# Kernel optimization log

Measured on AMD Instinct MI355X. Metric: run time of the kernel, lower is better.

## Reference

```python
import jax, jax.numpy as jnp
import numpy as np


def _discretize(A, B, C, step):
    # Bilinear (Tustin) discretization, as in the source module.
    N = A.shape[0]
    I = jnp.eye(N, dtype=A.dtype)
    BL = jnp.linalg.inv(I - (step / 2.0) * A)
    Ab = BL @ (I + (step / 2.0) * A)
    Bb = (BL * step) @ B  # (N, 1)
    return Ab, Bb, C


def _k_conv(Ab, Bb, Cb, L):
    # K[l] = Cb @ Ab^l @ Bb, computed by a linear recurrence instead of
    # L explicit matrix powers (same math as the source's K_conv).
    def step(v, _):
        k = (Cb @ v)[0, 0]
        return Ab @ v, k

    _, K = jax.lax.scan(step, Bb, None, length=L)
    return K  # (L,)


def setup_inputs() -> dict:
    key = jax.random.key(0)
    k_u, k_a, k_b, k_c, k_s = jax.random.split(key, 5)
    N, L, BATCH = 64, 16384, 512
    u = jax.random.normal(k_u, (BATCH, L), dtype=jnp.float32)
    # lecun_normal inits: std = 1/sqrt(fan_in)
    A = jax.random.normal(k_a, (N, N), dtype=jnp.float32) / np.sqrt(N)
    B = jax.random.normal(k_b, (N, 1), dtype=jnp.float32)  # fan_in = 1
    C = jax.random.normal(k_c, (1, N), dtype=jnp.float32) / np.sqrt(N)
    D = jnp.ones((1,), dtype=jnp.float32)
    # log_step_initializer(dt_min=1e-3, dt_max=0.1)
    lo, hi = np.log(1e-3), np.log(0.1)
    log_step = (jax.random.uniform(k_s, (1,)) * (hi - lo) + lo).astype(jnp.float32)
    return {"u": u, "A": A, "B": B, "C": C, "D": D, "log_step": log_step}


def reference(u, A, B, C, D, log_step) -> jnp.ndarray:
    L = u.shape[-1]
    step = jnp.exp(log_step)  # (1,)
    Ab, Bb, Cb = _discretize(A, B, C, step)
    K = _k_conv(Ab, Bb, Cb, L)  # (L,)
    # FFT causal convolution: pad both signals to length 2L (as in source),
    # multiply in frequency domain, take first L samples.
    n = 2 * L
    ud = jnp.fft.rfft(u, n=n, axis=-1)          # (BATCH, L+1) complex
    Kd = jnp.fft.rfft(K, n=n)                   # (L+1,) complex, broadcast
    y = jnp.fft.irfft(ud * Kd, n=n, axis=-1)[..., :L]
    return y + D * u
```

## Files before the change

kernel.cpp:

```cpp
#include <hip/hip_runtime.h>
#include <cstddef>

typedef double f64x4 __attribute__((ext_vector_type(4)));
typedef float  f32x4 __attribute__((ext_vector_type(4)));
typedef short  bf16x8 __attribute__((ext_vector_type(8)));

static constexpr int RCN = 512 * 128;

static constexpr size_t WS_W  = 0;
static constexpr size_t WS_G  = 8192;
static constexpr size_t WS_MD = 32768;
static constexpr size_t WS_BV = 40960;
static constexpr size_t WS_X  = WS_BV + (size_t)RCN * 64;

__device__ __forceinline__ unsigned short f2bf(float f) {
  union { float f; unsigned u; } v; v.f = f;
  unsigned u = v.u + 0x7FFFu + ((v.u >> 16) & 1u);
  return (unsigned short)(u >> 16);
}

__device__ __forceinline__ double probeE(int i, int k) {
  return (double)(((i * 3 + k * 5) & 7) - 3);
}
__device__ __forceinline__ double probeF(int k, int j) {
  return (double)(((k * 7 + j * 2) & 7) - 4);
}

__device__ __forceinline__ bool probe_mfma_layout(int lr, int lq, int rowm[4], int* colm_out)
{
  f64x4 z; z[0] = 0.0; z[1] = 0.0; z[2] = 0.0; z[3] = 0.0;
  f64x4 p1 = __builtin_amdgcn_mfma_f64_16x16x4f64((double)lr, 1.0, z, 0, 0, 0);
  f64x4 p2 = __builtin_amdgcn_mfma_f64_16x16x4f64(1.0, (double)lr, z, 0, 0, 0);
  bool okl = true;
#pragma unroll
  for (int r = 0; r < 4; ++r) {
    int rr = (int)(p1[r] * 0.25 + 0.5);
    okl = okl && (p1[r] == 4.0 * (double)rr) && rr >= 0 && rr < 16;
    rowm[r] = rr & 15;
    okl = okl && (p2[r] == p2[0]);
  }
  int cc = (int)(p2[0] * 0.25 + 0.5);
  okl = okl && (p2[0] == 4.0 * (double)cc) && cc >= 0 && cc < 16;
  *colm_out = cc & 15;
  f64x4 d = __builtin_amdgcn_mfma_f64_16x16x4f64(probeE(lr, lq), probeF(lq, lr), z, 0, 0, 0);
#pragma unroll
  for (int r = 0; r < 4; ++r) {
    double ref = 0.0;
#pragma unroll
    for (int k = 0; k < 4; ++k) ref += probeE(rowm[r], k) * probeF(k, cc & 15);
    okl = okl && (d[r] == ref);
  }
  return __all(okl) != 0;
}

template<bool ADD>
__device__ __forceinline__ void mm64_mfma(const double* A, const double* B, double* D,
                                          int wi, int wj, int lr, int lq,
                                          const int rowm[4], int colm)
{
  f64x4 acc;
  if (ADD) {
#pragma unroll
    for (int r = 0; r < 4; ++r)
      acc[r] = D[(wi * 16 + rowm[r]) * 65 + wj * 16 + colm];
  } else {
    acc[0] = 0.0; acc[1] = 0.0; acc[2] = 0.0; acc[3] = 0.0;
  }
#pragma unroll
  for (int kb = 0; kb < 16; ++kb) {
    double a = A[(wi * 16 + lr) * 65 + kb * 4 + lq];
    double b = B[(kb * 4 + lq) * 65 + wj * 16 + lr];
    acc = __builtin_amdgcn_mfma_f64_16x16x4f64(a, b, acc, 0, 0, 0);
  }
  __syncthreads();
#pragma unroll
  for (int r = 0; r < 4; ++r)
    D[(wi * 16 + rowm[r]) * 65 + wj * 16 + colm] = acc[r];
  __syncthreads();
}

__device__ __forceinline__ void wh_tile(const float* Wf, const float* Hf,
                                        const double* Pd, float* Wo, float* Ho,
                                        int n, bool isW, int wi, int wj,
                                        int lr, int lq, const int rowm[4], int colm)
{
  f64x4 acc;
  acc[0] = 0.0; acc[1] = 0.0; acc[2] = 0.0; acc[3] = 0.0;
#pragma unroll
  for (int kb = 0; kb < 16; ++kb) {
    double a, b;
    if (isW) {
      a = (double)Wf[(wi * 16 + lr) * 65 + kb * 4 + lq];
      b = Pd[(wj * 16 + lr) * 65 + kb * 4 + lq];
    } else {
      a = (double)Hf[(wi * 16 + lr) * 65 + kb * 4 + lq];
      b = Pd[(kb * 4 + lq) * 65 + wj * 16 + lr];
    }
    acc = __builtin_amdgcn_mfma_f64_16x16x4f64(a, b, acc, 0, 0, 0);
  }
#pragma unroll
  for (int r = 0; r < 4; ++r) {
    int drow = wi * 16 + rowm[r];
    if (drow < n) {
      if (isW) Wo[(n + drow) * 65 + wj * 16 + colm] = (float)acc[r];
      else     Ho[(n + drow) * 65 + wj * 16 + colm] = (float)acc[r];
    }
  }
}

template<bool ADD>
__device__ __forceinline__ void mm64x2(const double* A, const double* B, double* D,
                                       int tr2, int tc2)
{
  double a00 = 0, a01 = 0, a10 = 0, a11 = 0;
#pragma unroll 8
  for (int c = 0; c < 64; ++c) {
    double av0 = A[(tr2 + 0) * 65 + c];
    double av1 = A[(tr2 + 1) * 65 + c];
    double bv0 = B[c * 65 + tc2 + 0];
    double bv1 = B[c * 65 + tc2 + 1];
    a00 = fma(av0, bv0, a00); a01 = fma(av0, bv1, a01);
    a10 = fma(av1, bv0, a10); a11 = fma(av1, bv1, a11);
  }
  double o00, o01, o10, o11;
  if (ADD) {
    o00 = D[(tr2 + 0) * 65 + tc2 + 0]; o01 = D[(tr2 + 0) * 65 + tc2 + 1];
    o10 = D[(tr2 + 1) * 65 + tc2 + 0]; o11 = D[(tr2 + 1) * 65 + tc2 + 1];
  }
  __syncthreads();
  D[(tr2 + 0) * 65 + tc2 + 0] = ADD ? (o00 + a00) : a00;
  D[(tr2 + 0) * 65 + tc2 + 1] = ADD ? (o01 + a01) : a01;
  D[(tr2 + 1) * 65 + tc2 + 0] = ADD ? (o10 + a10) : a10;
  D[(tr2 + 1) * 65 + tc2 + 1] = ADD ? (o11 + a11) : a11;
  __syncthreads();
}

__global__ __launch_bounds__(1024) void k_precomp(
    const float* __restrict__ Ain, const float* __restrict__ Bin,
    const float* __restrict__ Cin, const float* __restrict__ Din,
    const float* __restrict__ LS, float* ws)
{
  __shared__ double Xd[64 * 65];
  __shared__ double Pd[64 * 65];
  __shared__ float  Wf[128 * 65];
  __shared__ float  Hf[128 * 65];
  __shared__ float  Kf[128];

  const int t    = threadIdx.x;
  const int wave = t >> 6;
  const int lane = t & 63;
  const int lr   = lane & 15;
  const int lq   = lane >> 4;
  const int wv_i = wave >> 2;
  const int wv_j = wave & 3;
  const int tr2  = (t >> 5) << 1;
  const int tc2  = (t & 31) << 1;

  int rowm[4]; int colm;
  const bool use_mfma = probe_mfma_layout(lr, lq, rowm, &colm);

  unsigned short* Wtg = (unsigned short*)(ws + WS_W);
  unsigned short* Gtg = (unsigned short*)(ws + WS_G);
  float* Mf = ws + WS_MD;

  const double step = exp((double)LS[0]);
  const double h = 0.5 * step;

  for (int idx = t; idx < 4096; idx += 1024) {
    int i = idx >> 6, j = idx & 63;
    double a = h * (double)Ain[idx];
    Xd[i * 65 + j] = a;
    Pd[i * 65 + j] = a + ((i == j) ? 1.0 : 0.0);
  }
  __syncthreads();

  if (use_mfma) {
    for (int k = 0; k < 3; ++k) {
      mm64_mfma<false>(Xd, Xd, Xd, wv_i, wv_j, lr, lq, rowm, colm);
      mm64_mfma<true >(Pd, Xd, Pd, wv_i, wv_j, lr, lq, rowm, colm);
    }
  } else {
    for (int k = 0; k < 3; ++k) {
      mm64x2<false>(Xd, Xd, Xd, tr2, tc2);
      mm64x2<true >(Pd, Xd, Pd, tr2, tc2);
    }
  }

  if (t < 64) {
    double bb = 0.0;
    for (int c = 0; c < 64; ++c) bb = fma(Pd[t * 65 + c], (double)Bin[c], bb);
    Wf[t] = (float)(bb * step);
  }
  __syncthreads();

  for (int idx = t; idx < 4096; idx += 1024) {
    int i = idx >> 6, j = idx & 63;
    Pd[i * 65 + j] = 2.0 * Pd[i * 65 + j] - ((i == j) ? 1.0 : 0.0);
  }
  __syncthreads();

  if (t < 64) {
    double hh = 0.0;
    for (int c = 0; c < 64; ++c) hh = fma((double)Cin[c], Pd[c * 65 + t], hh);
    Hf[t] = (float)hh;
  }
  __syncthreads();

  if (use_mfma) {
    for (int k = 0; k < 7; ++k) {
      const int n     = 1 << k;
      const int tpm   = (n + 15) >> 4;
      const int tiles = tpm << 2;
      if (tiles <= 8) {
        if (wave < 2 * tiles) {
          const bool isW = wave < tiles;
          const int  w   = isW ? wave : wave - tiles;
          wh_tile(Wf, Hf, Pd, Wf, Hf, n, isW, w >> 2, w & 3, lr, lq, rowm, colm);
        }
      } else {
        wh_tile(Wf, Hf, Pd, Wf, Hf, n, true,  wv_i, wv_j, lr, lq, rowm, colm);
        wh_tile(Wf, Hf, Pd, Wf, Hf, n, false, wv_i, wv_j, lr, lq, rowm, colm);
      }
      mm64_mfma<false>(Pd, Pd, Pd, wv_i, wv_j, lr, lq, rowm, colm);
    }
  } else {
    for (int k = 0; k < 7; ++k) {
      const int n = 1 << k;
      if (n <= 16) {
        if (t < (n << 6)) {
          int r = t >> 6, ii = t & 63;
          double aw = 0.0, ah = 0.0;
#pragma unroll 4
          for (int c = 0; c < 64; ++c) {
            aw = fma(Pd[ii * 65 + c], (double)Wf[r * 65 + c], aw);
            ah = fma((double)Hf[r * 65 + c], Pd[c * 65 + ii], ah);
          }
          Wf[(n + r) * 65 + ii] = (float)aw;
          Hf[(n + r) * 65 + ii] = (float)ah;
        }
      } else if (n == 32) {
        const int r  = t >> 5;
        const int i2 = (t & 31) << 1;
        double w0 = 0, w1 = 0, h0 = 0, h1 = 0;
#pragma unroll 4
        for (int c = 0; c < 64; ++c) {
          double wr = (double)Wf[r * 65 + c];
          w0 = fma(wr, Pd[(i2 + 0) * 65 + c], w0);
          w1 = fma(wr, Pd[(i2 + 1) * 65 + c], w1);
          double hr = (double)Hf[r * 65 + c];
          h0 = fma(hr, Pd[c * 65 + i2 + 0], h0);
          h1 = fma(hr, Pd[c * 65 + i2 + 1], h1);
        }
        Wf[(32 + r) * 65 + i2 + 0] = (float)w0;
        Wf[(32 + r) * 65 + i2 + 1] = (float)w1;
        Hf[(32 + r) * 65 + i2 + 0] = (float)h0;
        Hf[(32 + r) * 65 + i2 + 1] = (float)h1;
      } else {
        const int r2 = tr2, i2 = tc2;
        double w00 = 0, w01 = 0, w10 = 0, w11 = 0;
        double h00 = 0, h01 = 0, h10 = 0, h11 = 0;
#pragma unroll 4
        for (int c = 0; c < 64; ++c) {
          double wa = (double)Wf[(r2 + 0) * 65 + c];
          double wb = (double)Wf[(r2 + 1) * 65 + c];
          double p0 = Pd[(i2 + 0) * 65 + c];
          double p1 = Pd[(i2 + 1) * 65 + c];
          w00 = fma(wa, p0, w00); w01 = fma(wa, p1, w01);
          w10 = fma(wb, p0, w10); w11 = fma(wb, p1, w11);
          double ha = (double)Hf[(r2 + 0) * 65 + c];
          double hb = (double)Hf[(r2 + 1) * 65 + c];
          double q0 = Pd[c * 65 + i2 + 0];
          double q1 = Pd[c * 65 + i2 + 1];
          h00 = fma(ha, q0, h00); h01 = fma(ha, q1, h01);
          h10 = fma(hb, q0, h10); h11 = fma(hb, q1, h11);
        }
        Wf[(64 + r2 + 0) * 65 + i2 + 0] = (float)w00;
        Wf[(64 + r2 + 0) * 65 + i2 + 1] = (float)w01;
        Wf[(64 + r2 + 1) * 65 + i2 + 0] = (float)w10;
        Wf[(64 + r2 + 1) * 65 + i2 + 1] = (float)w11;
        Hf[(64 + r2 + 0) * 65 + i2 + 0] = (float)h00;
        Hf[(64 + r2 + 0) * 65 + i2 + 1] = (float)h01;
        Hf[(64 + r2 + 1) * 65 + i2 + 0] = (float)h10;
        Hf[(64 + r2 + 1) * 65 + i2 + 1] = (float)h11;
      }
      mm64x2<false>(Pd, Pd, Pd, tr2, tc2);
    }
  }

  for (int idx = t; idx < 4096; idx += 1024)
    Mf[idx] = (float)Pd[(idx >> 6) * 65 + (idx & 63)];

  if (use_mfma) mm64_mfma<false>(Pd, Pd, Pd, wv_i, wv_j, lr, lq, rowm, colm);
  else          mm64x2<false>(Pd, Pd, Pd, tr2, tc2);
  for (int idx = t; idx < 4096; idx += 1024)
    Mf[4096 + idx] = (float)Pd[(idx >> 6) * 65 + (idx & 63)];

  if (t < 128) {
    double s = 0.0;
    for (int c = 0; c < 64; ++c) s = fma((double)Cin[c], (double)Wf[t * 65 + c], s);
    Kf[t] = (float)s;
  }
  __syncthreads();

  for (int idx = t; idx < 8192; idx += 1024) {
    int i = idx >> 7, kk = idx & 127;
    Wtg[idx] = f2bf(Wf[(127 - kk) * 65 + i]);
  }

  const float Dval = Din[0];
  for (int idx = t; idx < 16384; idx += 1024) {
    int r = idx >> 7, kg = idx & 127;
    float v = (r >= kg) ? Kf[r - kg] : 0.f;
    if (kg == r) v += Dval;
    Gtg[r * 192 + kg] = f2bf(v);
  }
  for (int idx = t; idx < 8192; idx += 1024) {
    int r = idx >> 6, i = idx & 63;
    Gtg[r * 192 + 128 + i] = f2bf(Hf[r * 65 + i]);
  }
}

__global__ __launch_bounds__(256) void k_chunkvec(
    const float* __restrict__ u, const unsigned short* __restrict__ Wt,
    float* __restrict__ bout)
{
  __shared__ unsigned short Bs[64 * 136];
  __shared__ unsigned short As[128 * 40];
  const int t = threadIdx.x;
  const int rc0 = blockIdx.x << 7;
  const int w  = t >> 6;
  const int lane = t & 63;
  const int lr = lane & 15, lq = lane >> 4;

  {
    const unsigned* src = (const unsigned*)Wt;
    unsigned* dst = (unsigned*)Bs;
    for (int idx = t; idx < 4096; idx += 256) {
      int r = idx >> 6, c = idx & 63;
      dst[r * 68 + c] = src[idx];
    }
  }
  for (int it = t; it < 1024; it += 256) {
    int rcl = it >> 3, k4 = (it & 7) << 2;
    float4 v = *(const float4*)&u[((size_t)(rc0 + rcl) << 7) + k4];
    ushort4 s;
    s.x = f2bf(v.x); s.y = f2bf(v.y); s.z = f2bf(v.z); s.w = f2bf(v.w);
    *(ushort4*)&As[rcl * 40 + k4] = s;
  }
  __syncthreads();

  f32x4 acc[2][4];
#pragma unroll
  for (int i = 0; i < 2; ++i)
#pragma unroll
    for (int j = 0; j < 4; ++j) { acc[i][j][0] = 0.f; acc[i][j][1] = 0.f; acc[i][j][2] = 0.f; acc[i][j][3] = 0.f; }

  for (int sl = 0; sl < 4; ++sl) {
    bf16x8 av[2], bv[4];
#pragma unroll
    for (int ti = 0; ti < 2; ++ti)
      av[ti] = *(const bf16x8*)&As[(w * 32 + ti * 16 + lr) * 40 + lq * 8];
#pragma unroll
    for (int tj = 0; tj < 4; ++tj)
      bv[tj] = *(const bf16x8*)&Bs[(tj * 16 + lr) * 136 + sl * 32 + lq * 8];
#pragma unroll
    for (int ti = 0; ti < 2; ++ti)
#pragma unroll
      for (int tj = 0; tj < 4; ++tj)
        acc[ti][tj] = __builtin_amdgcn_mfma_f32_16x16x32_bf16(av[ti], bv[tj], acc[ti][tj], 0, 0, 0);
    if (sl < 3) {
      __syncthreads();
      for (int it = t; it < 1024; it += 256) {
        int rcl = it >> 3, k4 = (it & 7) << 2;
        float4 v = *(const float4*)&u[((size_t)(rc0 + rcl) << 7) + ((sl + 1) << 5) + k4];
        ushort4 s;
        s.x = f2bf(v.x); s.y = f2bf(v.y); s.z = f2bf(v.z); s.w = f2bf(v.w);
        *(ushort4*)&As[rcl * 40 + k4] = s;
      }
      __syncthreads();
    }
  }

#pragma unroll
  for (int ti = 0; ti < 2; ++ti)
#pragma unroll
    for (int tj = 0; tj < 4; ++tj)
#pragma unroll
      for (int r = 0; r < 4; ++r) {
        int row = rc0 + w * 32 + ti * 16 + lq * 4 + r;
        bout[((size_t)row << 6) + tj * 16 + lr] = acc[ti][tj][r];
      }
}

__global__ __launch_bounds__(256) void k_scan(
    const float* __restrict__ Mf,
    const float* __restrict__ bv, float* __restrict__ Xg)
{
  __shared__ float bs[128 * 64];
  __shared__ float ds[64 * 64];
  __shared__ float xs[64 * 64];
  const int t = threadIdx.x, w = t >> 6, lane = t & 63;
  const float* br = bv + ((size_t)blockIdx.x << 13);
  float* Xr = Xg + ((size_t)blockIdx.x << 13);

  for (int it = t; it < 2048; it += 256)
    ((float4*)bs)[it] = ((const float4*)br)[it];

  float Mr[64], M2r[64];
#pragma unroll
  for (int c4 = 0; c4 < 16; ++c4) {
    *(float4*)&Mr[c4 * 4]  = *(const float4*)&Mf[(lane << 6) + c4 * 4];
    *(float4*)&M2r[c4 * 4] = *(const float4*)&Mf[4096 + (lane << 6) + c4 * 4];
  }
  __syncthreads();

  for (int k = 0; k < 16; ++k) {
    const int tp = (w << 4) + k;
    float y0 = 0.f, y1 = 0.f, y2 = 0.f, y3 = 0.f;
#pragma unroll
    for (int c4 = 0; c4 < 16; ++c4) {
      float4 bb = *(const float4*)&bs[((tp << 1) << 6) + (c4 << 2)];
      y0 = fmaf(Mr[c4 * 4 + 0], bb.x, y0);
      y1 = fmaf(Mr[c4 * 4 + 1], bb.y, y1);
      y2 = fmaf(Mr[c4 * 4 + 2], bb.z, y2);
      y3 = fmaf(Mr[c4 * 4 + 3], bb.w, y3);
    }
    ds[(tp << 6) + lane] = ((y0 + y1) + (y2 + y3)) + bs[(((tp << 1) + 1) << 6) + lane];
  }
  __syncthreads();

  if (w == 0) {
    float x = 0.f;
    float ecur = ds[lane];
    for (int u = 0; u < 64; ++u) {
      xs[(u << 6) + lane] = x;
      float en = (u < 63) ? ds[((u + 1) << 6) + lane] : 0.f;
      const unsigned xb = __float_as_uint(x);
      float y0 = 0.f, y1 = 0.f, y2 = 0.f, y3 = 0.f;
#pragma unroll
      for (int c = 0; c < 64; c += 4) {
        y0 = fmaf(M2r[c + 0], __uint_as_float(__builtin_amdgcn_readlane(xb, c + 0)), y0);
        y1 = fmaf(M2r[c + 1], __uint_as_float(__builtin_amdgcn_readlane(xb, c + 1)), y1);
        y2 = fmaf(M2r[c + 2], __uint_as_float(__builtin_amdgcn_readlane(xb, c + 2)), y2);
        y3 = fmaf(M2r[c + 3], __uint_as_float(__builtin_amdgcn_readlane(xb, c + 3)), y3);
      }
      x = ((y0 + y1) + (y2 + y3)) + ecur;
      ecur = en;
    }
  }
  __syncthreads();

  for (int k = 0; k < 16; ++k) {
    const int tp = (w << 4) + k;
    Xr[((tp << 1) << 6) + lane] = xs[(tp << 6) + lane];
    float y0 = 0.f, y1 = 0.f, y2 = 0.f, y3 = 0.f;
#pragma unroll
    for (int c4 = 0; c4 < 16; ++c4) {
      float4 xx = *(const float4*)&xs[(tp << 6) + (c4 << 2)];
      y0 = fmaf(Mr[c4 * 4 + 0], xx.x, y0);
      y1 = fmaf(Mr[c4 * 4 + 1], xx.y, y1);
      y2 = fmaf(Mr[c4 * 4 + 2], xx.z, y2);
      y3 = fmaf(Mr[c4 * 4 + 3], xx.w, y3);
    }
    Xr[(((tp << 1) + 1) << 6) + lane] =
        ((y0 + y1) + (y2 + y3)) + bs[((tp << 1) << 6) + lane];
  }
}

__global__ __launch_bounds__(256) void k_main(
    const float* __restrict__ u, const float* __restrict__ Xg,
    const unsigned short* __restrict__ Gt, float* __restrict__ out)
{
  __shared__ unsigned short Gs[128 * 200];
  __shared__ unsigned short As[128 * 40];
  const int t = threadIdx.x;
  const int rc0 = blockIdx.x << 7;
  const int w  = t >> 6;
  const int lane = t & 63;
  const int lr = lane & 15, lq = lane >> 4;

  {
    const unsigned* src = (const unsigned*)Gt;
    unsigned* dst = (unsigned*)Gs;
    for (int idx = t; idx < 12288; idx += 256) {
      int r = idx / 96, c = idx - r * 96;
      dst[r * 100 + c] = src[idx];
    }
  }
  for (int it = t; it < 1024; it += 256) {
    int rcl = it >> 3, k4 = (it & 7) << 2;
    float4 v = *(const float4*)&u[((size_t)(rc0 + rcl) << 7) + k4];
    ushort4 s;
    s.x = f2bf(v.x); s.y = f2bf(v.y); s.z = f2bf(v.z); s.w = f2bf(v.w);
    *(ushort4*)&As[rcl * 40 + k4] = s;
  }
  __syncthreads();

  f32x4 acc[2][8];
#pragma unroll
  for (int i = 0; i < 2; ++i)
#pragma unroll
    for (int j = 0; j < 8; ++j) { acc[i][j][0] = 0.f; acc[i][j][1] = 0.f; acc[i][j][2] = 0.f; acc[i][j][3] = 0.f; }

  for (int sl = 0; sl < 6; ++sl) {
    bf16x8 av[2], bv[8];
#pragma unroll
    for (int ti = 0; ti < 2; ++ti)
      av[ti] = *(const bf16x8*)&As[(w * 32 + ti * 16 + lr) * 40 + lq * 8];
#pragma unroll
    for (int tj = 0; tj < 8; ++tj)
      bv[tj] = *(const bf16x8*)&Gs[(tj * 16 + lr) * 200 + sl * 32 + lq * 8];
#pragma unroll
    for (int ti = 0; ti < 2; ++ti)
#pragma unroll
      for (int tj = 0; tj < 8; ++tj)
        acc[ti][tj] = __builtin_amdgcn_mfma_f32_16x16x32_bf16(av[ti], bv[tj], acc[ti][tj], 0, 0, 0);
    if (sl < 5) {
      __syncthreads();
      for (int it = t; it < 1024; it += 256) {
        int rcl = it >> 3, k4 = (it & 7) << 2;
        int kg = ((sl + 1) << 5) + k4;
        float4 v;
        if (kg < 128)
          v = *(const float4*)&u[((size_t)(rc0 + rcl) << 7) + kg];
        else
          v = *(const float4*)&Xg[((size_t)(rc0 + rcl) << 6) + (kg - 128)];
        ushort4 s;
        s.x = f2bf(v.x); s.y = f2bf(v.y); s.z = f2bf(v.z); s.w = f2bf(v.w);
        *(ushort4*)&As[rcl * 40 + k4] = s;
      }
      __syncthreads();
    }
  }

#pragma unroll
  for (int ti = 0; ti < 2; ++ti)
#pragma unroll
    for (int tj = 0; tj < 8; ++tj)
#pragma unroll
      for (int r = 0; r < 4; ++r) {
        int row = rc0 + w * 32 + ti * 16 + lq * 4 + r;
        out[((size_t)row << 7) + tj * 16 + lr] = acc[ti][tj][r];
      }
}

extern "C" void kernel_launch(void* const* d_in, const int* in_sizes, int n_in,
                              void* d_out, int out_size, void* d_ws, size_t ws_size,
                              hipStream_t stream) {
  (void)in_sizes; (void)n_in; (void)out_size; (void)ws_size;
  const float* u  = (const float*)d_in[0];
  const float* A  = (const float*)d_in[1];
  const float* Bv = (const float*)d_in[2];
  const float* Cv = (const float*)d_in[3];
  const float* Dv = (const float*)d_in[4];
  const float* ls = (const float*)d_in[5];
  float* out = (float*)d_out;
  float* ws  = (float*)d_ws;

  k_precomp<<<1, 1024, 0, stream>>>(A, Bv, Cv, Dv, ls, ws);
  k_chunkvec<<<512, 256, 0, stream>>>(u, (const unsigned short*)(ws + WS_W), ws + WS_BV);
  k_scan<<<512, 256, 0, stream>>>(ws + WS_MD, ws + WS_BV, ws + WS_X);
  k_main<<<512, 256, 0, stream>>>(u, ws + WS_X, (const unsigned short*)(ws + WS_G), out);
}
```

Baseline: 211.1 us.

## Fuse chunk-vector, scan, and main GEMM kernels into one per-row kernel

Merges the three per-batch-row kernels (chunk state projection, inter-chunk scan, output GEMM) into a single kernel that keeps the intermediate chunk vectors and scanned states in LDS, aliasing buffers across phases. It removes the global round-trips for the b-vectors and X states and two kernel launches. In exchange it uses about 77KB of LDS per block, limiting occupancy, and the serial single-wave scan now sits inside the same block as the GEMMs, with no overlap across kernels.

New measurement: 188.6 us. 1.12x faster.

```diff
diff --git a/kernel.cpp b/kernel.cpp
--- a/kernel.cpp
+++ b/kernel.cpp
@@ -320,228 +320,198 @@
   }
 }
 
-__global__ __launch_bounds__(256) void k_chunkvec(
+__global__ __launch_bounds__(256, 2) void k_fused(
     const float* __restrict__ u, const unsigned short* __restrict__ Wt,
-    float* __restrict__ bout)
+    const unsigned short* __restrict__ Gt, const float* __restrict__ Mf,
+    float* __restrict__ out)
 {
-  __shared__ unsigned short Bs[64 * 136];
-  __shared__ unsigned short As[128 * 40];
-  const int t = threadIdx.x;
-  const int rc0 = blockIdx.x << 7;
-  const int w  = t >> 6;
+  __shared__ __align__(16) unsigned char Lds[78848];
+  float*          bs  = (float*)(Lds);
+  unsigned short* WtS = (unsigned short*)(Lds + 34816);
+  float*          dsb = (float*)(Lds + 34816);
+  unsigned short* Gs  = (unsigned short*)(Lds);
+  unsigned short* As  = (unsigned short*)(Lds + 52224);
+  float*          xs  = (float*)(Lds + 62464);
+  unsigned short* Xbf = (unsigned short*)(Lds + 62464);
+
+  const int t    = threadIdx.x;
+  const int w    = t >> 6;
   const int lane = t & 63;
-  const int lr = lane & 15, lq = lane >> 4;
+  const int lr   = lane & 15, lq = lane >> 4;
+  const int row  = blockIdx.x;
+  const float* urow = u + ((size_t)row << 14);
+  float* orow = out + ((size_t)row << 14);
+
+  auto stageA = [&](int k0) {
+    for (int it = t; it < 1024; it += 256) {
+      int rcl = it >> 3, k4 = (it & 7) << 2;
+      float4 v = *(const float4*)&urow[(rcl << 7) + k0 + k4];
+      ushort4 s;
+      s.x = f2bf(v.x); s.y = f2bf(v.y); s.z = f2bf(v.z); s.w = f2bf(v.w);
+      *(ushort4*)&As[rcl * 40 + k4] = s;
+    }
+  };
 
   {
-    const unsigned* src = (const unsigned*)Wt;
-    unsigned* dst = (unsigned*)Bs;
+    const unsigned* srcW = (const unsigned*)Wt;
+    unsigned* dstW = (unsigned*)WtS;
     for (int idx = t; idx < 4096; idx += 256) {
       int r = idx >> 6, c = idx & 63;
-      dst[r * 68 + c] = src[idx];
-    }
-  }
-  for (int it = t; it < 1024; it += 256) {
-    int rcl = it >> 3, k4 = (it & 7) << 2;
-    float4 v = *(const float4*)&u[((size_t)(rc0 + rcl) << 7) + k4];
-    ushort4 s;
-    s.x = f2bf(v.x); s.y = f2bf(v.y); s.z = f2bf(v.z); s.w = f2bf(v.w);
-    *(ushort4*)&As[rcl * 40 + k4] = s;
-  }
-  __syncthreads();
-
-  f32x4 acc[2][4];
-#pragma unroll
-  for (int i = 0; i < 2; ++i)
-#pragma unroll
-    for (int j = 0; j < 4; ++j) { acc[i][j][0] = 0.f; acc[i][j][1] = 0.f; acc[i][j][2] = 0.f; acc[i][j][3] = 0.f; }
-
-  for (int sl = 0; sl < 4; ++sl) {
-    bf16x8 av[2], bv[4];
+      dstW[r * 68 + c] = srcW[idx];
+    }
+    stageA(0);
+    __syncthreads();
+
+    f32x4 acc[2][4];
+#pragma unroll
+    for (int i = 0; i < 2; ++i)
+#pragma unroll
+      for (int j = 0; j < 4; ++j) { acc[i][j][0] = 0.f; acc[i][j][1] = 0.f; acc[i][j][2] = 0.f; acc[i][j][3] = 0.f; }
+
+    for (int sl = 0; sl < 4; ++sl) {
+      bf16x8 av[2], bv[4];
+#pragma unroll
+      for (int ti = 0; ti < 2; ++ti)
+        av[ti] = *(const bf16x8*)&As[(w * 32 + ti * 16 + lr) * 40 + lq * 8];
+#pragma unroll
+      for (int tj = 0; tj < 4; ++tj)
+        bv[tj] = *(const bf16x8*)&WtS[(tj * 16 + lr) * 136 + sl * 32 + lq * 8];
+#pragma unroll
+      for (int ti = 0; ti < 2; ++ti)
+#pragma unroll
+        for (int tj = 0; tj < 4; ++tj)
+          acc[ti][tj] = __builtin_amdgcn_mfma_f32_16x16x32_bf16(av[ti], bv[tj], acc[ti][tj], 0, 0, 0);
+      if (sl < 3) {
+        __syncthreads();
+        stageA((sl + 1) << 5);
+        __syncthreads();
+      }
+    }
 #pragma unroll
     for (int ti = 0; ti < 2; ++ti)
-      av[ti] = *(const bf16x8*)&As[(w * 32 + ti * 16 + lr) * 40 + lq * 8];
-#pragma unroll
-    for (int tj = 0; tj < 4; ++tj)
-      bv[tj] = *(const bf16x8*)&Bs[(tj * 16 + lr) * 136 + sl * 32 + lq * 8];
-#pragma unroll
-    for (int ti = 0; ti < 2; ++ti)
 #pragma unroll
       for (int tj = 0; tj < 4; ++tj)
-        acc[ti][tj] = __builtin_amdgcn_mfma_f32_16x16x32_bf16(av[ti], bv[tj], acc[ti][tj], 0, 0, 0);
-    if (sl < 3) {
-      __syncthreads();
-      for (int it = t; it < 1024; it += 256) {
-        int rcl = it >> 3, k4 = (it & 7) << 2;
-        float4 v = *(const float4*)&u[((size_t)(rc0 + rcl) << 7) + ((sl + 1) << 5) + k4];
-        ushort4 s;
-        s.x = f2bf(v.x); s.y = f2bf(v.y); s.z = f2bf(v.z); s.w = f2bf(v.w);
-        *(ushort4*)&As[rcl * 40 + k4] = s;
-      }
-      __syncthreads();
-    }
-  }
-
-#pragma unroll
-  for (int ti = 0; ti < 2; ++ti)
-#pragma unroll
-    for (int tj = 0; tj < 4; ++tj)
-#pragma unroll
-      for (int r = 0; r < 4; ++r) {
-        int row = rc0 + w * 32 + ti * 16 + lq * 4 + r;
-        bout[((size_t)row << 6) + tj * 16 + lr] = acc[ti][tj][r];
-      }
-}
-
-__global__ __launch_bounds__(256) void k_scan(
-    const float* __restrict__ Mf,
-    const float* __restrict__ bv, float* __restrict__ Xg)
-{
-  __shared__ float bs[128 * 64];
-  __shared__ float ds[64 * 64];
-  __shared__ float xs[64 * 64];
-  const int t = threadIdx.x, w = t >> 6, lane = t & 63;
-  const float* br = bv + ((size_t)blockIdx.x << 13);
-  float* Xr = Xg + ((size_t)blockIdx.x << 13);
-
-  for (int it = t; it < 2048; it += 256)
-    ((float4*)bs)[it] = ((const float4*)br)[it];
-
-  float Mr[64], M2r[64];
-#pragma unroll
-  for (int c4 = 0; c4 < 16; ++c4) {
-    *(float4*)&Mr[c4 * 4]  = *(const float4*)&Mf[(lane << 6) + c4 * 4];
-    *(float4*)&M2r[c4 * 4] = *(const float4*)&Mf[4096 + (lane << 6) + c4 * 4];
-  }
-  __syncthreads();
-
-  for (int k = 0; k < 16; ++k) {
-    const int tp = (w << 4) + k;
-    float y0 = 0.f, y1 = 0.f, y2 = 0.f, y3 = 0.f;
-#pragma unroll
-    for (int c4 = 0; c4 < 16; ++c4) {
-      float4 bb = *(const float4*)&bs[((tp << 1) << 6) + (c4 << 2)];
-      y0 = fmaf(Mr[c4 * 4 + 0], bb.x, y0);
-      y1 = fmaf(Mr[c4 * 4 + 1], bb.y, y1);
-      y2 = fmaf(Mr[c4 * 4 + 2], bb.z, y2);
-      y3 = fmaf(Mr[c4 * 4 + 3], bb.w, y3);
-    }
-    ds[(tp << 6) + lane] = ((y0 + y1) + (y2 + y3)) + bs[(((tp << 1) + 1) << 6) + lane];
-  }
-  __syncthreads();
-
-  if (w == 0) {
-    float x = 0.f;
-    float ecur = ds[lane];
-    for (int u = 0; u < 64; ++u) {
-      xs[(u << 6) + lane] = x;
-      float en = (u < 63) ? ds[((u + 1) << 6) + lane] : 0.f;
-      const unsigned xb = __float_as_uint(x);
+#pragma unroll
+        for (int r = 0; r < 4; ++r)
+          bs[(w * 32 + ti * 16 + lq * 4 + r) * 68 + tj * 16 + lr] = acc[ti][tj][r];
+    __syncthreads();
+  }
+
+  {
+    float Mr[64];
+#pragma unroll
+    for (int c4 = 0; c4 < 16; ++c4)
+      *(float4*)&Mr[c4 * 4] = *(const float4*)&Mf[(lane << 6) + c4 * 4];
+
+    for (int k = 0; k < 16; ++k) {
+      const int tp = (w << 4) + k;
       float y0 = 0.f, y1 = 0.f, y2 = 0.f, y3 = 0.f;
 #pragma unroll
-      for (int c = 0; c < 64; c += 4) {
-        y0 = fmaf(M2r[c + 0], __uint_as_float(__builtin_amdgcn_readlane(xb, c + 0)), y0);
-        y1 = fmaf(M2r[c + 1], __uint_as_float(__builtin_amdgcn_readlane(xb, c + 1)), y1);
-        y2 = fmaf(M2r[c + 2], __uint_as_float(__builtin_amdgcn_readlane(xb, c + 2)), y2);
-        y3 = fmaf(M2r[c + 3], __uint_as_float(__builtin_amdgcn_readlane(xb, c + 3)), y3);
-      }
-      x = ((y0 + y1) + (y2 + y3)) + ecur;
-      ecur = en;
-    }
-  }
-  __syncthreads();
-
-  for (int k = 0; k < 16; ++k) {
-    const int tp = (w << 4) + k;
-    Xr[((tp << 1) << 6) + lane] = xs[(tp << 6) + lane];
-    float y0 = 0.f, y1 = 0.f, y2 = 0.f, y3 = 0.f;
-#pragma unroll
-    for (int c4 = 0; c4 < 16; ++c4) {
-      float4 xx = *(const float4*)&xs[(tp << 6) + (c4 << 2)];
-      y0 = fmaf(Mr[c4 * 4 + 0], xx.x, y0);
-      y1 = fmaf(Mr[c4 * 4 + 1], xx.y, y1);
-      y2 = fmaf(Mr[c4 * 4 + 2], xx.z, y2);
-      y3 = fmaf(Mr[c4 * 4 + 3], xx.w, y3);
-    }
-    Xr[(((tp << 1) + 1) << 6) + lane] =
-        ((y0 + y1) + (y2 + y3)) + bs[((tp << 1) << 6) + lane];
-  }
-}
-
-__global__ __launch_bounds__(256) void k_main(
-    const float* __restrict__ u, const float* __restrict__ Xg,
-    const unsigned short* __restrict__ Gt, float* __restrict__ out)
-{
-  __shared__ unsigned short Gs[128 * 200];
-  __shared__ unsigned short As[128 * 40];
-  const int t = threadIdx.x;
-  const int rc0 = blockIdx.x << 7;
-  const int w  = t >> 6;
-  const int lane = t & 63;
-  const int lr = lane & 15, lq = lane >> 4;
+      for (int c4 = 0; c4 < 16; ++c4) {
+        float4 bb = *(const float4*)&bs[(tp << 1) * 68 + (c4 << 2)];
+        y0 = fmaf(Mr[c4 * 4 + 0], bb.x, y0);
+        y1 = fmaf(Mr[c4 * 4 + 1], bb.y, y1);
+        y2 = fmaf(Mr[c4 * 4 + 2], bb.z, y2);
+        y3 = fmaf(Mr[c4 * 4 + 3], bb.w, y3);
+      }
+      dsb[tp * 68 + lane] = ((y0 + y1) + (y2 + y3)) + bs[((tp << 1) + 1) * 68 + lane];
+    }
+    __syncthreads();
+
+    if (w == 0) {
+      float M2r[64];
+#pragma unroll
+      for (int c4 = 0; c4 < 16; ++c4)
+        *(float4*)&M2r[c4 * 4] = *(const float4*)&Mf[4096 + (lane << 6) + c4 * 4];
+      float x = 0.f;
+      float ecur = dsb[lane];
+      for (int u2 = 0; u2 < 64; ++u2) {
+        xs[(u2 << 6) + lane] = x;
+        float en = (u2 < 63) ? dsb[(u2 + 1) * 68 + lane] : 0.f;
+        const unsigned xb = __float_as_uint(x);
+        float y0 = 0.f, y1 = 0.f, y2 = 0.f, y3 = 0.f;
+#pragma unroll
+        for (int c = 0; c < 64; c += 4) {
+          y0 = fmaf(M2r[c + 0], __uint_as_float(__builtin_amdgcn_readlane(xb, c + 0)), y0);
+          y1 = fmaf(M2r[c + 1], __uint_as_float(__builtin_amdgcn_readlane(xb, c + 1)), y1);
+          y2 = fmaf(M2r[c + 2], __uint_as_float(__builtin_amdgcn_readlane(xb, c + 2)), y2);
+          y3 = fmaf(M2r[c + 3], __uint_as_float(__builtin_amdgcn_readlane(xb, c + 3)), y3);
+        }
+        x = ((y0 + y1) + (y2 + y3)) + ecur;
+        ecur = en;
+      }
+    }
+    __syncthreads();
+
+    for (int k = 0; k < 16; ++k) {
+      const int tp = (w << 4) + k;
+      float y0 = 0.f, y1 = 0.f, y2 = 0.f, y3 = 0.f;
+#pragma unroll
+      for (int c4 = 0; c4 < 16; ++c4) {
+        float4 xx = *(const float4*)&xs[(tp << 6) + (c4 << 2)];
+        y0 = fmaf(Mr[c4 * 4 + 0], xx.x, y0);
+        y1 = fmaf(Mr[c4 * 4 + 1], xx.y, y1);
+        y2 = fmaf(Mr[c4 * 4 + 2], xx.z, y2);
+        y3 = fmaf(Mr[c4 * 4 + 3], xx.w, y3);
+      }
+      float xeven = xs[(tp << 6) + lane];
+      float xodd  = ((y0 + y1) + (y2 + y3)) + bs[(tp << 1) * 68 + lane];
+      Xbf[((tp << 1) + 0) * 64 + lane] = f2bf(xeven);
+      Xbf[((tp << 1) + 1) * 64 + lane] = f2bf(xodd);
+    }
+    __syncthreads();
+  }
 
   {
-    const unsigned* src = (const unsigned*)Gt;
-    unsigned* dst = (unsigned*)Gs;
+    const unsigned* srcG = (const unsigned*)Gt;
+    unsigned* dstG = (unsigned*)Gs;
     for (int idx = t; idx < 12288; idx += 256) {
       int r = idx / 96, c = idx - r * 96;
-      dst[r * 100 + c] = src[idx];
-    }
-  }
-  for (int it = t; it < 1024; it += 256) {
-    int rcl = it >> 3, k4 = (it & 7) << 2;
-    float4 v = *(const float4*)&u[((size_t)(rc0 + rcl) << 7) + k4];
-    ushort4 s;
-    s.x = f2bf(v.x); s.y = f2bf(v.y); s.z = f2bf(v.z); s.w = f2bf(v.w);
-    *(ushort4*)&As[rcl * 40 + k4] = s;
-  }
-  __syncthreads();
-
-  f32x4 acc[2][8];
-#pragma unroll
-  for (int i = 0; i < 2; ++i)
-#pragma unroll
-    for (int j = 0; j < 8; ++j) { acc[i][j][0] = 0.f; acc[i][j][1] = 0.f; acc[i][j][2] = 0.f; acc[i][j][3] = 0.f; }
-
-  for (int sl = 0; sl < 6; ++sl) {
-    bf16x8 av[2], bv[8];
+      dstG[r * 100 + c] = srcG[idx];
+    }
+    stageA(0);
+    __syncthreads();
+
+    f32x4 acc[2][8];
+#pragma unroll
+    for (int i = 0; i < 2; ++i)
+#pragma unroll
+      for (int j = 0; j < 8; ++j) { acc[i][j][0] = 0.f; acc[i][j][1] = 0.f; acc[i][j][2] = 0.f; acc[i][j][3] = 0.f; }
+
+    for (int sl = 0; sl < 6; ++sl) {
+      bf16x8 av[2], bv[8];
+#pragma unroll
+      for (int ti = 0; ti < 2; ++ti) {
+        if (sl < 4)
+          av[ti] = *(const bf16x8*)&As[(w * 32 + ti * 16 + lr) * 40 + lq * 8];
+        else
+          av[ti] = *(const bf16x8*)&Xbf[(w * 32 + ti * 16 + lr) * 64 + (sl - 4) * 32 + lq * 8];
+      }
+#pragma unroll
+      for (int tj = 0; tj < 8; ++tj)
+        bv[tj] = *(const bf16x8*)&Gs[(tj * 16 + lr) * 200 + sl * 32 + lq * 8];
+#pragma unroll
+      for (int ti = 0; ti < 2; ++ti)
+#pragma unroll
+        for (int tj = 0; tj < 8; ++tj)
+          acc[ti][tj] = __builtin_amdgcn_mfma_f32_16x16x32_bf16(av[ti], bv[tj], acc[ti][tj], 0, 0, 0);
+      if (sl < 3) {
+        __syncthreads();
+        stageA((sl + 1) << 5);
+        __syncthreads();
+      }
+    }
+
 #pragma unroll
     for (int ti = 0; ti < 2; ++ti)
-      av[ti] = *(const bf16x8*)&As[(w * 32 + ti * 16 + lr) * 40 + lq * 8];
-#pragma unroll
-    for (int tj = 0; tj < 8; ++tj)
-      bv[tj] = *(const bf16x8*)&Gs[(tj * 16 + lr) * 200 + sl * 32 + lq * 8];
-#pragma unroll
-    for (int ti = 0; ti < 2; ++ti)
 #pragma unroll
       for (int tj = 0; tj < 8; ++tj)
-        acc[ti][tj] = __builtin_amdgcn_mfma_f32_16x16x32_bf16(av[ti], bv[tj], acc[ti][tj], 0, 0, 0);
-    if (sl < 5) {
-      __syncthreads();
-      for (int it = t; it < 1024; it += 256) {
-        int rcl = it >> 3, k4 = (it & 7) << 2;
-        int kg = ((sl + 1) << 5) + k4;
-        float4 v;
-        if (kg < 128)
-          v = *(const float4*)&u[((size_t)(rc0 + rcl) << 7) + kg];
-        else
-          v = *(const float4*)&Xg[((size_t)(rc0 + rcl) << 6) + (kg - 128)];
-        ushort4 s;
-        s.x = f2bf(v.x); s.y = f2bf(v.y); s.z = f2bf(v.z); s.w = f2bf(v.w);
-        *(ushort4*)&As[rcl * 40 + k4] = s;
-      }
-      __syncthreads();
-    }
-  }
-
-#pragma unroll
-  for (int ti = 0; ti < 2; ++ti)
-#pragma unroll
-    for (int tj = 0; tj < 8; ++tj)
-#pragma unroll
-      for (int r = 0; r < 4; ++r) {
-        int row = rc0 + w * 32 + ti * 16 + lq * 4 + r;
-        out[((size_t)row << 7) + tj * 16 + lr] = acc[ti][tj][r];
-      }
+#pragma unroll
+        for (int r = 0; r < 4; ++r) {
+          int rcl = w * 32 + ti * 16 + lq * 4 + r;
+          orow[((size_t)rcl << 7) + tj * 16 + lr] = acc[ti][tj][r];
+        }
+  }
 }
 
 extern "C" void kernel_launch(void* const* d_in, const int* in_sizes, int n_in,
@@ -558,7 +528,7 @@
   float* ws  = (float*)d_ws;
 
   k_precomp<<<1, 1024, 0, stream>>>(A, Bv, Cv, Dv, ls, ws);
-  k_chunkvec<<<512, 256, 0, stream>>>(u, (const unsigned short*)(ws + WS_W), ws + WS_BV);
-  k_scan<<<512, 256, 0, stream>>>(ws + WS_MD, ws + WS_BV, ws + WS_X);
-  k_main<<<512, 256, 0, stream>>>(u, ws + WS_X, (const unsigned short*)(ws + WS_G), out);
-}
+  k_fused<<<512, 256, 0, stream>>>(u, (const unsigned short*)(ws + WS_W),
+                                   (const unsigned short*)(ws + WS_G),
+                                   ws + WS_MD, out);
+}
```
